# Performance work log

Hardware: AMD Instinct MI355X
Metric: run time of the kernel (lower is better)

## Reference

```python
import jax, jax.numpy as jnp
import numpy as np
from jax import lax

B, N, C = 8, 4096, 512
NH, R = 8, 8
HD = C // NH
EPS = 1e-3  # keras LayerNormalization default epsilon


def setup_inputs() -> dict:
    key = jax.random.key(0)
    ks = jax.random.split(key, 8)
    s = 0.02
    x = jax.random.normal(ks[0], (B, N, C), dtype=jnp.float32)
    Wq = jax.random.normal(ks[1], (C, C), dtype=jnp.float32) * s
    Wkv = jax.random.normal(ks[2], (C, 2 * C), dtype=jnp.float32) * s
    conv_w = jax.random.normal(ks[3], (R, R, C, C), dtype=jnp.float32) * s  # HWIO
    gamma = jnp.ones((C,), dtype=jnp.float32)
    beta = jnp.zeros((C,), dtype=jnp.float32)
    Wp = jax.random.normal(ks[4], (C, C), dtype=jnp.float32) * s
    bp = jnp.zeros((C,), dtype=jnp.float32)
    return {"x": x, "Wq": Wq, "Wkv": Wkv, "conv_w": conv_w,
            "gamma": gamma, "beta": beta, "Wp": Wp, "bp": bp}


def reference(x, Wq, Wkv, conv_w, gamma, beta, Wp, bp):
    b, n, c = x.shape
    h = w = int(np.sqrt(n))
    scale = 1.0 / np.sqrt(float(HD))

    # queries: Rearrange 'b n (hd nh) -> b n nh hd' then 'b n nh hd -> b nh n hd'
    q = x @ Wq                                   # [B, N, C]
    q = q.reshape(b, n, HD, NH).transpose(0, 3, 1, 2)  # [B, NH, N, HD]

    # spatial reduction of K/V: strided conv (SAME) + layernorm
    fmap = x.reshape(b, h, w, c)
    fmap = lax.conv_general_dilated(
        fmap, conv_w, window_strides=(R, R), padding="SAME",
        dimension_numbers=("NHWC", "HWIO", "NHWC"))   # [B, h/R, w/R, C]
    m = fmap.shape[1] * fmap.shape[2]
    fmap = fmap.reshape(b, m, c)
    mu = jnp.mean(fmap, axis=-1, keepdims=True)
    var = jnp.var(fmap, axis=-1, keepdims=True)
    fmap = (fmap - mu) * lax.rsqrt(var + EPS) * gamma + beta

    # key/value: Rearrange 'b m (f nh hd) -> b m f nh hd', perm [2,0,3,1,4]
    kv = fmap @ Wkv                              # [B, M, 2C]
    kv = kv.reshape(b, m, 2, NH, HD).transpose(2, 0, 3, 1, 4)  # [2, B, NH, M, HD]
    k, v = kv[0], kv[1]

    attn = jax.nn.softmax(jnp.einsum("bhnd,bhmd->bhnm", q, k) * scale, axis=-1)
    out = jnp.einsum("bhnm,bhmd->bhnd", attn, v)  # [B, NH, N, HD]
    out = out.transpose(0, 2, 1, 3).reshape(b, n, c)  # 'b n h c -> b n (h c)'
    return out @ Wp + bp
```

## Files before the change

kernel.cpp:

```cpp
#include <hip/hip_runtime.h>

typedef unsigned short u16;
typedef __bf16 bf16x8 __attribute__((ext_vector_type(8)));
typedef float floatx4 __attribute__((ext_vector_type(4)));

__device__ __forceinline__ u16 f2bf(float f) {
    unsigned u = __float_as_uint(f);
    u += 0x7fff + ((u >> 16) & 1);
    return (u16)(u >> 16);
}

#define GLOAD_LDS16(g, l) __builtin_amdgcn_global_load_lds( \
    (const __attribute__((address_space(1))) void*)(g),      \
    (__attribute__((address_space(3))) void*)(l), 16, 0, 0)

__global__ void cast_f32_bf16(const float* __restrict__ in, u16* __restrict__ out) {
    size_t o = ((size_t)blockIdx.x * 256 + threadIdx.x) * 4;
    float4 v = *(const float4*)(in + o);
    unsigned w0 = (unsigned)f2bf(v.x) | ((unsigned)f2bf(v.y) << 16);
    unsigned w1 = (unsigned)f2bf(v.z) | ((unsigned)f2bf(v.w) << 16);
    *(uint2*)(out + o) = make_uint2(w0, w1);
}

__global__ void transpose_cast(const float* __restrict__ in, u16* __restrict__ out,
                               int R, int Cn) {
    __shared__ float tile[32][33];
    int c0 = blockIdx.x * 32, r0 = blockIdx.y * 32;
    int tx = threadIdx.x, ty = threadIdx.y;
    #pragma unroll
    for (int yy = 0; yy < 4; ++yy)
        tile[ty + yy * 8][tx] = in[(size_t)(r0 + ty + yy * 8) * Cn + c0 + tx];
    __syncthreads();
    #pragma unroll
    for (int yy = 0; yy < 4; ++yy)
        out[(size_t)(c0 + ty + yy * 8) * R + r0 + tx] = f2bf(tile[tx][ty + yy * 8]);
}

template<int MODE, int ASRC>
__global__ __launch_bounds__(256) void gemm_bt(
    const u16* __restrict__ A, const u16* __restrict__ B, float* __restrict__ out,
    int M, int N, int K, int KC, const float* __restrict__ bias)
{
    __shared__ u16 As[128 * 32];
    __shared__ u16 Bs[128 * 32];
    const int tid = threadIdx.x;
    const int wv = tid >> 6, lane = tid & 63;
    const int quad = lane >> 4, l15 = lane & 15;
    const int bm = blockIdx.y * 128, bn = blockIdx.x * 128;
    const int k0 = blockIdx.z * KC;
    const int wr = wv >> 1, wc = wv & 1;

    floatx4 acc[4][4];
    #pragma unroll
    for (int i = 0; i < 4; ++i)
        #pragma unroll
        for (int j = 0; j < 4; ++j)
            acc[i][j] = (floatx4){0.f, 0.f, 0.f, 0.f};

    for (int kt = 0; kt < KC; kt += 32) {
        const int kk = k0 + kt;
        #pragma unroll
        for (int c2 = 0; c2 < 2; ++c2) {
            int e = ((wv * 2 + c2) * 64 + lane) * 8;
            int row = e >> 5, col = e & 31;
            if (ASRC == 0) {
                const u16* ga = A + (size_t)(bm + row) * K + kk + col;
                GLOAD_LDS16(ga, &As[(wv * 2 + c2) * 512]);
            } else {
                int p = bm + row;
                int b = p >> 6, ij = p & 63, ii = ij >> 3, jj = ij & 7;
                int r12 = kk >> 9, r1 = r12 >> 3, r2 = r12 & 7;
                int n = (ii * 8 + r1) * 64 + jj * 8 + r2;
                const u16* ga = A + ((size_t)(b * 4096 + n)) * 512 + (kk & 511) + col;
                GLOAD_LDS16(ga, &As[(wv * 2 + c2) * 512]);
            }
            const u16* gb = B + (size_t)(bn + row) * K + kk + col;
            GLOAD_LDS16(gb, &Bs[(wv * 2 + c2) * 512]);
        }
        __syncthreads();
        bf16x8 af[4], bfr[4];
        #pragma unroll
        for (int i = 0; i < 4; ++i)
            af[i] = *(const bf16x8*)&As[(wr * 64 + i * 16 + l15) * 32 + quad * 8];
        #pragma unroll
        for (int j = 0; j < 4; ++j)
            bfr[j] = *(const bf16x8*)&Bs[(wc * 64 + j * 16 + l15) * 32 + quad * 8];
        #pragma unroll
        for (int i = 0; i < 4; ++i)
            #pragma unroll
            for (int j = 0; j < 4; ++j)
                acc[i][j] = __builtin_amdgcn_mfma_f32_16x16x32_bf16(af[i], bfr[j], acc[i][j], 0, 0, 0);
        __syncthreads();
    }

    #pragma unroll
    for (int i = 0; i < 4; ++i) {
        #pragma unroll
        for (int j = 0; j < 4; ++j) {
            #pragma unroll
            for (int r = 0; r < 4; ++r) {
                int m = bm + wr * 64 + i * 16 + quad * 4 + r;
                int n = bn + wc * 64 + j * 16 + l15;
                float v = acc[i][j][r];
                if (MODE == 0) {
                    out[(size_t)blockIdx.z * 262144 + (size_t)m * N + n] = v;
                } else if (MODE == 1) {
                    int b = m >> 12, nn = m & 4095;
                    int h = n & 7, d = n >> 3;
                    ((u16*)out)[((size_t)((b * 8 + h) * 4096 + nn)) * 64 + d] = f2bf(v);
                } else if (MODE == 2) {
                    int b = m >> 6, mm = m & 63;
                    int f = n >> 9, c = n & 511, h = c >> 6, d = c & 63;
                    size_t idx;
                    if (f == 0) idx = ((size_t)((b * 8 + h) * 64 + mm)) * 64 + d;
                    else        idx = 262144 + ((size_t)((b * 8 + h) * 64 + d)) * 64 + mm;
                    atomicAdd(&out[idx], v);
                } else {
                    out[(size_t)m * 512 + n] = v + bias[n];
                }
            }
        }
    }
}

__global__ __launch_bounds__(256) void reduce_ln_bf16(
    const float* __restrict__ part, u16* __restrict__ out,
    const float* __restrict__ gamma, const float* __restrict__ beta)
{
    int row = blockIdx.x, tid = threadIdx.x;
    const float* base = part + (size_t)row * 512 + tid * 2;
    float2 v = {0.f, 0.f};
    #pragma unroll
    for (int z = 0; z < 32; ++z) {
        float2 t = *(const float2*)(base + (size_t)z * 262144);
        v.x += t.x; v.y += t.y;
    }
    float s = v.x + v.y, ss = v.x * v.x + v.y * v.y;
    #pragma unroll
    for (int off = 32; off > 0; off >>= 1) {
        s  += __shfl_down(s, off);
        ss += __shfl_down(ss, off);
    }
    __shared__ float red[8];
    __shared__ float stats[2];
    int wvi = tid >> 6, lane = tid & 63;
    if (lane == 0) { red[wvi * 2] = s; red[wvi * 2 + 1] = ss; }
    __syncthreads();
    if (tid == 0) {
        float S = red[0] + red[2] + red[4] + red[6];
        float SS = red[1] + red[3] + red[5] + red[7];
        float mean = S * (1.f / 512.f);
        float var = SS * (1.f / 512.f) - mean * mean;
        stats[0] = mean; stats[1] = rsqrtf(var + 1e-3f);
    }
    __syncthreads();
    float mean = stats[0], rstd = stats[1];
    float o0 = (v.x - mean) * rstd * gamma[tid * 2]     + beta[tid * 2];
    float o1 = (v.y - mean) * rstd * gamma[tid * 2 + 1] + beta[tid * 2 + 1];
    unsigned w = (unsigned)f2bf(o0) | ((unsigned)f2bf(o1) << 16);
    *(unsigned*)&out[(size_t)row * 512 + tid * 2] = w;
}

__global__ __launch_bounds__(256) void attn_mfma(
    const u16* __restrict__ qbf, const float* __restrict__ kvf, u16* __restrict__ attn_out)
{
    __shared__ u16 Ksh[64 * 64];
    __shared__ u16 Vt[64 * 64];
    __shared__ u16 Psh[4][32 * 64];
    const int bh = blockIdx.x, qt = blockIdx.y;
    const int tid = threadIdx.x;
    const int wv = tid >> 6, lane = tid & 63;
    const int quad = lane >> 4, l15 = lane & 15;

    {
        const float* kb = kvf + (size_t)bh * 4096;
        const float* vb = kvf + 262144 + (size_t)bh * 4096;
        for (int t = tid; t < 2048; t += 256) {
            float2 a = ((const float2*)kb)[t];
            ((unsigned*)Ksh)[t] = (unsigned)f2bf(a.x) | ((unsigned)f2bf(a.y) << 16);
            float2 b2 = ((const float2*)vb)[t];
            ((unsigned*)Vt)[t] = (unsigned)f2bf(b2.x) | ((unsigned)f2bf(b2.y) << 16);
        }
    }
    __syncthreads();

    const u16* qb = qbf + ((size_t)bh * 4096 + qt * 128 + wv * 32) * 64;
    bf16x8 qf[2][2];
    #pragma unroll
    for (int i = 0; i < 2; ++i)
        #pragma unroll
        for (int ks = 0; ks < 2; ++ks)
            qf[i][ks] = *(const bf16x8*)(qb + (i * 16 + l15) * 64 + ks * 32 + quad * 8);

    floatx4 s[2][4];
    #pragma unroll
    for (int i = 0; i < 2; ++i)
        #pragma unroll
        for (int j = 0; j < 4; ++j)
            s[i][j] = (floatx4){0.f, 0.f, 0.f, 0.f};
    #pragma unroll
    for (int j = 0; j < 4; ++j) {
        #pragma unroll
        for (int ks = 0; ks < 2; ++ks) {
            bf16x8 kf = *(const bf16x8*)&Ksh[(j * 16 + l15) * 64 + ks * 32 + quad * 8];
            #pragma unroll
            for (int i = 0; i < 2; ++i)
                s[i][j] = __builtin_amdgcn_mfma_f32_16x16x32_bf16(qf[i][ks], kf, s[i][j], 0, 0, 0);
        }
    }

    u16* P = Psh[wv];
    float rs[2][4];
    #pragma unroll
    for (int i = 0; i < 2; ++i)
        #pragma unroll
        for (int r = 0; r < 4; ++r) rs[i][r] = 0.f;
    #pragma unroll
    for (int i = 0; i < 2; ++i)
        #pragma unroll
        for (int j = 0; j < 4; ++j)
            #pragma unroll
            for (int r = 0; r < 4; ++r) {
                float e = __expf(s[i][j][r] * 0.125f);
                rs[i][r] += e;
                P[(i * 16 + quad * 4 + r) * 64 + j * 16 + l15] = f2bf(e);
            }
    #pragma unroll
    for (int m = 1; m < 16; m <<= 1)
        #pragma unroll
        for (int i = 0; i < 2; ++i)
            #pragma unroll
            for (int r = 0; r < 4; ++r)
                rs[i][r] += __shfl_xor(rs[i][r], m);
    __syncthreads();

    floatx4 o[2][4];
    #pragma unroll
    for (int i = 0; i < 2; ++i)
        #pragma unroll
        for (int j = 0; j < 4; ++j)
            o[i][j] = (floatx4){0.f, 0.f, 0.f, 0.f};
    #pragma unroll
    for (int ks = 0; ks < 2; ++ks) {
        bf16x8 pf[2];
        #pragma unroll
        for (int i = 0; i < 2; ++i)
            pf[i] = *(const bf16x8*)&P[(i * 16 + l15) * 64 + ks * 32 + quad * 8];
        #pragma unroll
        for (int j = 0; j < 4; ++j) {
            bf16x8 vf = *(const bf16x8*)&Vt[(j * 16 + l15) * 64 + ks * 32 + quad * 8];
            #pragma unroll
            for (int i = 0; i < 2; ++i)
                o[i][j] = __builtin_amdgcn_mfma_f32_16x16x32_bf16(pf[i], vf, o[i][j], 0, 0, 0);
        }
    }

    const int b = bh >> 3, h = bh & 7;
    #pragma unroll
    for (int i = 0; i < 2; ++i) {
        #pragma unroll
        for (int r = 0; r < 4; ++r) {
            float inv = 1.f / rs[i][r];
            int n = qt * 128 + wv * 32 + i * 16 + quad * 4 + r;
            u16* op = attn_out + ((size_t)(b * 4096 + n)) * 512 + h * 64;
            #pragma unroll
            for (int j = 0; j < 4; ++j)
                op[j * 16 + l15] = f2bf(o[i][j][r] * inv);
        }
    }
}

extern "C" void kernel_launch(void* const* d_in, const int* in_sizes, int n_in,
                              void* d_out, int out_size, void* d_ws, size_t ws_size,
                              hipStream_t stream) {
    const float* x      = (const float*)d_in[0];
    const float* Wq     = (const float*)d_in[1];
    const float* Wkv    = (const float*)d_in[2];
    const float* conv_w = (const float*)d_in[3];
    const float* gamma  = (const float*)d_in[4];
    const float* beta   = (const float*)d_in[5];
    const float* Wp     = (const float*)d_in[6];
    const float* bp     = (const float*)d_in[7];
    float* out = (float*)d_out;

    char* w = (char*)d_ws;
    const size_t MB = 1ull << 20;
    u16*   x_bf      = (u16*)(w + 0);
    u16*   WconvT    = (u16*)(w + 32 * MB);
    u16*   WqT       = (u16*)(w + 64 * MB);
    u16*   WkvT      = (u16*)(w + 65 * MB);
    u16*   WpT       = (u16*)(w + 66 * MB);
    u16*   q_bf      = (u16*)(w + 67 * MB);
    float* fmap_part = (float*)(w + 99 * MB);
    u16*   fmap_ln   = (u16*)(w + 131 * MB);
    float* kv_f      = (float*)(w + 132 * MB);
    u16*   attn_bf   = (u16*)(w + 134 * MB);

    hipMemsetAsync(kv_f, 0, 2 * 262144 * 4, stream);

    cast_f32_bf16<<<16384, 256, 0, stream>>>(x, x_bf);
    transpose_cast<<<dim3(16, 16),   dim3(32, 8), 0, stream>>>(Wq,     WqT,    512,   512);
    transpose_cast<<<dim3(32, 16),   dim3(32, 8), 0, stream>>>(Wkv,    WkvT,   512,   1024);
    transpose_cast<<<dim3(16, 1024), dim3(32, 8), 0, stream>>>(conv_w, WconvT, 32768, 512);
    transpose_cast<<<dim3(16, 16),   dim3(32, 8), 0, stream>>>(Wp,     WpT,    512,   512);

    gemm_bt<1, 0><<<dim3(4, 256, 1), 256, 0, stream>>>(x_bf, WqT, (float*)q_bf, 32768, 512, 512, 512, nullptr);
    gemm_bt<0, 1><<<dim3(4, 4, 32), 256, 0, stream>>>(x_bf, WconvT, fmap_part, 512, 512, 32768, 1024, nullptr);
    reduce_ln_bf16<<<512, 256, 0, stream>>>(fmap_part, fmap_ln, gamma, beta);
    gemm_bt<2, 0><<<dim3(8, 4, 4), 256, 0, stream>>>(fmap_ln, WkvT, kv_f, 512, 1024, 512, 128, nullptr);
    attn_mfma<<<dim3(64, 32), 256, 0, stream>>>(q_bf, kv_f, attn_bf);
    gemm_bt<3, 0><<<dim3(4, 256, 1), 256, 0, stream>>>(attn_bf, WpT, out, 32768, 512, 512, 512, bp);
}
```

Measured before the change: 385.0 us.

## Permute Wq columns, deepen GEMM K-step to 64, double conv split-K

Three changes ship together. First, the Q weight is transposed with a column permutation so the Q GEMM epilogue writes head-contiguous output, giving coalesced stores instead of stride-8 scattered bf16 writes. Second, the GEMM main loop now loads two 32-wide K slices per barrier pair, halving the number of __syncthreads per K and doubling LDS use. Third, the conv GEMM split-K goes from 32 to 64 slices for more parallelism on the 512x512 output, at the cost of twice as many partials to write and reduce, so the workspace layout is shifted.

```diff
diff --git a/kernel.cpp b/kernel.cpp
--- a/kernel.cpp
+++ b/kernel.cpp
@@ -36,13 +36,29 @@
         out[(size_t)(c0 + ty + yy * 8) * R + r0 + tx] = f2bf(tile[tx][ty + yy * 8]);
 }
 
+__global__ void transpose_cast_qperm(const float* __restrict__ in, u16* __restrict__ out) {
+    __shared__ float tile[32][33];
+    int c0 = blockIdx.x * 32, r0 = blockIdx.y * 32;
+    int tx = threadIdx.x, ty = threadIdx.y;
+    #pragma unroll
+    for (int yy = 0; yy < 4; ++yy)
+        tile[ty + yy * 8][tx] = in[(size_t)(r0 + ty + yy * 8) * 512 + c0 + tx];
+    __syncthreads();
+    #pragma unroll
+    for (int yy = 0; yy < 4; ++yy) {
+        int cc = c0 + ty + yy * 8;
+        int np = (cc & 7) * 64 + (cc >> 3);
+        out[(size_t)np * 512 + r0 + tx] = f2bf(tile[tx][ty + yy * 8]);
+    }
+}
+
 template<int MODE, int ASRC>
 __global__ __launch_bounds__(256) void gemm_bt(
     const u16* __restrict__ A, const u16* __restrict__ B, float* __restrict__ out,
     int M, int N, int K, int KC, const float* __restrict__ bias)
 {
-    __shared__ u16 As[128 * 32];
-    __shared__ u16 Bs[128 * 32];
+    __shared__ u16 As[2][128 * 32];
+    __shared__ u16 Bs[2][128 * 32];
     const int tid = threadIdx.x;
     const int wv = tid >> 6, lane = tid & 63;
     const int quad = lane >> 4, l15 = lane & 15;
@@ -57,39 +73,46 @@
         for (int j = 0; j < 4; ++j)
             acc[i][j] = (floatx4){0.f, 0.f, 0.f, 0.f};
 
-    for (int kt = 0; kt < KC; kt += 32) {
+    for (int kt = 0; kt < KC; kt += 64) {
         const int kk = k0 + kt;
         #pragma unroll
-        for (int c2 = 0; c2 < 2; ++c2) {
-            int e = ((wv * 2 + c2) * 64 + lane) * 8;
-            int row = e >> 5, col = e & 31;
-            if (ASRC == 0) {
-                const u16* ga = A + (size_t)(bm + row) * K + kk + col;
-                GLOAD_LDS16(ga, &As[(wv * 2 + c2) * 512]);
-            } else {
-                int p = bm + row;
-                int b = p >> 6, ij = p & 63, ii = ij >> 3, jj = ij & 7;
-                int r12 = kk >> 9, r1 = r12 >> 3, r2 = r12 & 7;
-                int n = (ii * 8 + r1) * 64 + jj * 8 + r2;
-                const u16* ga = A + ((size_t)(b * 4096 + n)) * 512 + (kk & 511) + col;
-                GLOAD_LDS16(ga, &As[(wv * 2 + c2) * 512]);
+        for (int hf = 0; hf < 2; ++hf) {
+            #pragma unroll
+            for (int c2 = 0; c2 < 2; ++c2) {
+                int idx = ((wv * 2 + c2) * 64 + lane) * 8;
+                int row = idx >> 5, col = idx & 31;
+                int k = kk + hf * 32 + col;
+                if (ASRC == 0) {
+                    const u16* ga = A + (size_t)(bm + row) * K + k;
+                    GLOAD_LDS16(ga, &As[hf][(wv * 2 + c2) * 512]);
+                } else {
+                    int p = bm + row;
+                    int b = p >> 6, ij = p & 63, ii = ij >> 3, jj = ij & 7;
+                    int r12 = k >> 9, r1 = r12 >> 3, r2 = r12 & 7;
+                    int n = (ii * 8 + r1) * 64 + jj * 8 + r2;
+                    const u16* ga = A + ((size_t)(b * 4096 + n)) * 512 + (k & 511);
+                    GLOAD_LDS16(ga, &As[hf][(wv * 2 + c2) * 512]);
+                }
+                const u16* gb = B + (size_t)(bn + row) * K + k;
+                GLOAD_LDS16(gb, &Bs[hf][(wv * 2 + c2) * 512]);
             }
-            const u16* gb = B + (size_t)(bn + row) * K + kk + col;
-            GLOAD_LDS16(gb, &Bs[(wv * 2 + c2) * 512]);
         }
         __syncthreads();
-        bf16x8 af[4], bfr[4];
-        #pragma unroll
-        for (int i = 0; i < 4; ++i)
-            af[i] = *(const bf16x8*)&As[(wr * 64 + i * 16 + l15) * 32 + quad * 8];
-        #pragma unroll
-        for (int j = 0; j < 4; ++j)
-            bfr[j] = *(const bf16x8*)&Bs[(wc * 64 + j * 16 + l15) * 32 + quad * 8];
-        #pragma unroll
-        for (int i = 0; i < 4; ++i)
+        #pragma unroll
+        for (int ks = 0; ks < 2; ++ks) {
+            bf16x8 af[4], bfr[4];
+            #pragma unroll
+            for (int i = 0; i < 4; ++i)
+                af[i] = *(const bf16x8*)&As[ks][(wr * 64 + i * 16 + l15) * 32 + quad * 8];
             #pragma unroll
             for (int j = 0; j < 4; ++j)
-                acc[i][j] = __builtin_amdgcn_mfma_f32_16x16x32_bf16(af[i], bfr[j], acc[i][j], 0, 0, 0);
+                bfr[j] = *(const bf16x8*)&Bs[ks][(wc * 64 + j * 16 + l15) * 32 + quad * 8];
+            #pragma unroll
+            for (int i = 0; i < 4; ++i)
+                #pragma unroll
+                for (int j = 0; j < 4; ++j)
+                    acc[i][j] = __builtin_amdgcn_mfma_f32_16x16x32_bf16(af[i], bfr[j], acc[i][j], 0, 0, 0);
+        }
         __syncthreads();
     }
 
@@ -106,7 +129,7 @@
                     out[(size_t)blockIdx.z * 262144 + (size_t)m * N + n] = v;
                 } else if (MODE == 1) {
                     int b = m >> 12, nn = m & 4095;
-                    int h = n & 7, d = n >> 3;
+                    int h = n >> 6, d = n & 63;
                     ((u16*)out)[((size_t)((b * 8 + h) * 4096 + nn)) * 64 + d] = f2bf(v);
                 } else if (MODE == 2) {
                     int b = m >> 6, mm = m & 63;
@@ -130,8 +153,8 @@
     int row = blockIdx.x, tid = threadIdx.x;
     const float* base = part + (size_t)row * 512 + tid * 2;
     float2 v = {0.f, 0.f};
-    #pragma unroll
-    for (int z = 0; z < 32; ++z) {
+    #pragma unroll 8
+    for (int z = 0; z < 64; ++z) {
         float2 t = *(const float2*)(base + (size_t)z * 262144);
         v.x += t.x; v.y += t.y;
     }
@@ -287,25 +310,25 @@
     const size_t MB = 1ull << 20;
     u16*   x_bf      = (u16*)(w + 0);
     u16*   WconvT    = (u16*)(w + 32 * MB);
-    u16*   WqT       = (u16*)(w + 64 * MB);
+    u16*   WqTp      = (u16*)(w + 64 * MB);
     u16*   WkvT      = (u16*)(w + 65 * MB);
     u16*   WpT       = (u16*)(w + 66 * MB);
     u16*   q_bf      = (u16*)(w + 67 * MB);
     float* fmap_part = (float*)(w + 99 * MB);
-    u16*   fmap_ln   = (u16*)(w + 131 * MB);
-    float* kv_f      = (float*)(w + 132 * MB);
-    u16*   attn_bf   = (u16*)(w + 134 * MB);
+    u16*   fmap_ln   = (u16*)(w + 163 * MB);
+    float* kv_f      = (float*)(w + 164 * MB);
+    u16*   attn_bf   = (u16*)(w + 166 * MB);
 
     hipMemsetAsync(kv_f, 0, 2 * 262144 * 4, stream);
 
     cast_f32_bf16<<<16384, 256, 0, stream>>>(x, x_bf);
-    transpose_cast<<<dim3(16, 16),   dim3(32, 8), 0, stream>>>(Wq,     WqT,    512,   512);
+    transpose_cast_qperm<<<dim3(16, 16), dim3(32, 8), 0, stream>>>(Wq, WqTp);
     transpose_cast<<<dim3(32, 16),   dim3(32, 8), 0, stream>>>(Wkv,    WkvT,   512,   1024);
     transpose_cast<<<dim3(16, 1024), dim3(32, 8), 0, stream>>>(conv_w, WconvT, 32768, 512);
     transpose_cast<<<dim3(16, 16),   dim3(32, 8), 0, stream>>>(Wp,     WpT,    512,   512);
 
-    gemm_bt<1, 0><<<dim3(4, 256, 1), 256, 0, stream>>>(x_bf, WqT, (float*)q_bf, 32768, 512, 512, 512, nullptr);
-    gemm_bt<0, 1><<<dim3(4, 4, 32), 256, 0, stream>>>(x_bf, WconvT, fmap_part, 512, 512, 32768, 1024, nullptr);
+    gemm_bt<1, 0><<<dim3(4, 256, 1), 256, 0, stream>>>(x_bf, WqTp, (float*)q_bf, 32768, 512, 512, 512, nullptr);
+    gemm_bt<0, 1><<<dim3(4, 4, 64), 256, 0, stream>>>(x_bf, WconvT, fmap_part, 512, 512, 32768, 512, nullptr);
     reduce_ln_bf16<<<512, 256, 0, stream>>>(fmap_part, fmap_ln, gamma, beta);
     gemm_bt<2, 0><<<dim3(8, 4, 4), 256, 0, stream>>>(fmap_ln, WkvT, kv_f, 512, 1024, 512, 128, nullptr);
     attn_mfma<<<dim3(64, 32), 256, 0, stream>>>(q_bf, kv_f, attn_bf);
```

Measured after the change: 360.7 us. 6.3% less time.
